# Optimization experiments

Measured on AMD Instinct MI355X. Metric: run time of the kernel, lower is better.

## Reference

```python
import jax, jax.numpy as jnp
import numpy as np

B, T, D, V, SPK = 8, 4096, 512, 1024, 512
DECAY = 0.95
COARSE_SCALE = 0.2
RES_SCALE = 0.35
MAX_LS = 1.2
MAX_SIL = 0.35
COLD_RUNS = 2.0
MIN_DUR = 2.0


def gelu(x):
    return jax.nn.gelu(x, approximate=False)


def setup_inputs() -> dict:
    key = jax.random.key(0)
    ks = jax.random.split(key, 24)
    def n(k, shape, s=1.0):
        return jax.random.normal(k, shape, dtype=jnp.float32) * s
    inp = {}
    inp['content_units'] = jax.random.randint(ks[0], (B, T), 0, V)
    inp['log_anchor'] = n(ks[1], (B, T), 0.5) + 1.0
    inp['unit_mask'] = jax.random.randint(ks[2], (B, T), 0, 2)
    inp['sealed_mask'] = jax.random.randint(ks[3], (B, T), 0, 2)
    inp['silence_mask'] = jax.random.randint(ks[4], (B, T), 0, 2)
    inp['sep_hint'] = jax.random.uniform(ks[5], (B, T), dtype=jnp.float32)
    inp['edge_cue'] = jax.random.uniform(ks[6], (B, T), dtype=jnp.float32)
    inp['run_stability'] = jax.random.uniform(ks[7], (B, T), dtype=jnp.float32)
    inp['global_rate'] = n(ks[8], (B,), 0.1) + 1.0
    inp['local_rate_ema'] = n(ks[9], (B, 1), 0.1) + 1.0
    inp['spk_embed'] = n(ks[10], (B, SPK))
    s = 0.02
    inp['emb_table'] = n(ks[11], (V, D), s)
    inp['feat_W'] = n(ks[12], (5, D), s)      # scalar features -> dim
    inp['feat_b'] = jnp.zeros((D,), jnp.float32)
    inp['spk_W'] = n(ks[13], (SPK, D), s)
    inp['spk_b'] = jnp.zeros((D,), jnp.float32)
    inp['coarse_W1'] = n(ks[14], (D + 1, D), s)
    inp['coarse_b1'] = jnp.zeros((D,), jnp.float32)
    inp['coarse_W2'] = n(ks[15], (D, 1), s)
    inp['coarse_b2'] = jnp.zeros((1,), jnp.float32)
    inp['res_W1'] = n(ks[16], (2 * D + 1, D), s)
    inp['res_b1'] = jnp.zeros((D,), jnp.float32)
    inp['res_W2'] = n(ks[17], (D, 1), s)
    inp['res_b2'] = jnp.zeros((1,), jnp.float32)
    inp['src_rate_init'] = jnp.zeros((1,), jnp.float32)
    return inp


def _local_rate_scan(observed_log, speech_mask, init_rate):
    # Causal masked exponential-decay recurrence: emitted rate at t is the
    # state BEFORE observing step t (strictly causal); state only updates on
    # speech-commit steps.
    def step(rate, xs):
        obs, m = xs  # [B], [B]
        new = jnp.where(m > 0, DECAY * rate + (1.0 - DECAY) * obs, rate)
        return new, rate
    final, seq = jax.lax.scan(step, init_rate, (observed_log.T, speech_mask.T))
    return seq.T, final[:, None]  # [B,T], [B,1]


def reference(content_units, log_anchor, unit_mask, sealed_mask, silence_mask,
              sep_hint, edge_cue, run_stability, global_rate, local_rate_ema,
              spk_embed, emb_table, feat_W, feat_b, spk_W, spk_b,
              coarse_W1, coarse_b1, coarse_W2, coarse_b2,
              res_W1, res_b1, res_W2, res_b2, src_rate_init):
    f32 = jnp.float32
    mask = jnp.clip(unit_mask.astype(f32), 0.0, 1.0)
    sealed = jnp.clip(sealed_mask.astype(f32), 0.0, 1.0)
    silence = jnp.clip(silence_mask.astype(f32), 0.0, 1.0) * mask
    stability = jnp.clip(run_stability.astype(f32), 0.0, 1.0) * mask
    commit = mask * sealed
    sil_commit = commit * silence
    speech = commit * (1.0 - silence)

    la = log_anchor.astype(f32)
    rate_seq, rate_final = _local_rate_scan(la, speech, local_rate_ema[:, 0].astype(f32))

    # CausalUnitRunEncoder: token embedding + projection of per-step scalars
    feats = jnp.stack([la, rate_seq, silence, sep_hint.astype(f32), edge_cue.astype(f32)], axis=-1)  # [B,T,5]
    query = gelu(emb_table[content_units] + feats @ feat_W + feat_b) * mask[..., None]  # [B,T,D]

    grc = global_rate.astype(f32).reshape(-1, 1)[:, :1]  # [B,1]
    spk_ctx = jnp.tanh(spk_embed.astype(f32) @ spk_W + spk_b)  # [B,D]

    gsa = (grc - rate_seq) * commit  # global_shift_analytic [B,T]
    coarse_in = jnp.concatenate([spk_ctx, grc], axis=-1)  # [B,D+1]
    coarse_scalar = COARSE_SCALE * jnp.tanh((gelu(coarse_in @ coarse_W1 + coarse_b1) @ coarse_W2 + coarse_b2)[:, 0])  # [B]
    coarse_corr = coarse_scalar[:, None] * commit
    global_term = (gsa + coarse_corr) * commit

    # residual head: split first-layer weights to avoid materializing the concat
    Wq, Ws, wg = res_W1[:D], res_W1[D:2 * D], res_W1[2 * D]
    h = gelu(query @ Wq + (spk_ctx @ Ws)[:, None, :] + global_term[..., None] * wg + res_b1)  # [B,T,D]
    residual = RES_SCALE * jnp.tanh((h @ res_W2 + res_b2)[..., 0])  # [B,T]

    prefix_prev = jnp.maximum(jnp.cumsum(speech, axis=1) - speech, 0.0)
    cold_gate = jnp.clip(prefix_prev / COLD_RUNS, 0.0, 1.0)
    short_gate = jnp.clip((jnp.maximum(jnp.exp(la), 1.0) - 1.0) / max(1.0, MIN_DUR - 1.0), 0.0, 1.0)
    residual_gate = cold_gate * short_gate * stability * speech
    residual = residual * residual_gate

    pred_speech = jnp.clip(global_term + residual, -MAX_LS, MAX_LS) * speech
    pred_silence = jnp.clip(global_term, -MAX_SIL, MAX_SIL) * sil_commit
    pred = pred_speech + pred_silence  # unit_logstretch [B,T]
    return pred
```

## Files before the change

### kernel.cpp

```cpp
#include <hip/hip_runtime.h>
#include <hip/hip_bf16.h>

#define BB 8
#define TT 4096
#define DD 512
#define MM (BB*TT)
#define DECAYF 0.95f
#define OMDECAYF (1.0f - 0.95f)

typedef __attribute__((ext_vector_type(8))) short bf16x8;
typedef __attribute__((ext_vector_type(4))) float f32x4;

__device__ __forceinline__ float gelu_f(float x){
  return 0.5f * x * (1.0f + erff(x * 0.70710678118654752f));
}

__device__ __forceinline__ unsigned short f2bf(float x){
  unsigned u = __float_as_uint(x);
  unsigned r = (u + 0x7FFFu + ((u >> 16) & 1u)) >> 16;
  return (unsigned short)r;
}

__global__ __launch_bounds__(512) void pre_kernel(
    const float* __restrict__ spk_embed, const float* __restrict__ spk_W,
    const float* __restrict__ spk_b, const float* __restrict__ rW1,
    const float* __restrict__ la_g, const int* __restrict__ um,
    const int* __restrict__ sm, const int* __restrict__ zm,
    const float* __restrict__ stab_g, const float* __restrict__ lre,
    float* __restrict__ spk_ctx, unsigned short* __restrict__ wqt,
    float* __restrict__ rate_seq, float* __restrict__ rgate_a,
    int* __restrict__ active_list, int* __restrict__ acount)
{
  __shared__ float se[DD];
  __shared__ float red[8][64];
  __shared__ float tile[64][65];
  __shared__ float wAg[8], wBg[8], wSg[8];
  __shared__ int wcnt[8];
  int blk = blockIdx.x, t = threadIdx.x;
  int lane = t & 63, wid = t >> 6;

  if (blk < 64){
    int b = blk >> 3, d0 = (blk & 7) * 64;
    int dl = lane, ks = wid;
    se[t] = spk_embed[b*DD + t];
    __syncthreads();
    float a = 0.f;
    const float* wp = spk_W + (long)(ks*64)*DD + d0 + dl;
    #pragma unroll 8
    for (int k = 0; k < 64; ++k) a += se[ks*64 + k] * wp[(long)k*DD];
    red[ks][dl] = a;
    __syncthreads();
    if (t < 64){
      float s = spk_b[d0 + t];
      #pragma unroll
      for (int i = 0; i < 8; ++i) s += red[i][t];
      spk_ctx[b*DD + d0 + t] = tanhf(s);
    }
    return;
  }
  if (blk < 128){
    int tb = blk - 64;
    int nb = (tb & 7) * 64, kb = (tb >> 3) * 64;
    int tx = t & 63, ty = t >> 6;
    #pragma unroll
    for (int i = 0; i < 8; ++i){
      int k = ty + i*8;
      tile[k][tx] = rW1[(long)(kb + k)*DD + nb + tx];
    }
    __syncthreads();
    #pragma unroll
    for (int i = 0; i < 8; ++i){
      int nl = ty + i*8;
      wqt[(long)(nb + nl)*DD + kb + tx] = f2bf(tile[tx][nl]);
    }
    return;
  }

  int b = blk - 128;
  int base = b*TT + t*8;
  float4 la0 = *(const float4*)(la_g + base);
  float4 la1 = *(const float4*)(la_g + base + 4);
  int4 u0 = *(const int4*)(um + base), u1 = *(const int4*)(um + base + 4);
  int4 s0 = *(const int4*)(sm + base), s1 = *(const int4*)(sm + base + 4);
  int4 z0 = *(const int4*)(zm + base), z1 = *(const int4*)(zm + base + 4);
  float4 st0 = *(const float4*)(stab_g + base), st1 = *(const float4*)(stab_g + base + 4);
  float lav[8] = {la0.x,la0.y,la0.z,la0.w,la1.x,la1.y,la1.z,la1.w};
  int uv[8] = {u0.x,u0.y,u0.z,u0.w,u1.x,u1.y,u1.z,u1.w};
  int sv[8] = {s0.x,s0.y,s0.z,s0.w,s1.x,s1.y,s1.z,s1.w};
  int zv[8] = {z0.x,z0.y,z0.z,z0.w,z1.x,z1.y,z1.z,z1.w};
  float stv_[8] = {st0.x,st0.y,st0.z,st0.w,st1.x,st1.y,st1.z,st1.w};
  float spv[8], stv[8];

  float A = 1.f, Bv = 0.f, S = 0.f;
  #pragma unroll
  for (int i = 0; i < 8; ++i){
    float m = uv[i] > 0 ? 1.f : 0.f;
    float sealed = sv[i] > 0 ? 1.f : 0.f;
    float sil = (zv[i] > 0 ? 1.f : 0.f) * m;
    float speech = (m * sealed) * (1.f - sil);
    spv[i] = speech;
    stv[i] = fminf(fmaxf(stv_[i], 0.f), 1.f) * m;
    if (speech > 0.f){
      Bv = DECAYF*Bv + OMDECAYF*lav[i];
      A *= DECAYF;
      S += 1.f;
    }
  }
  #pragma unroll
  for (int d = 1; d < 64; d <<= 1){
    float Au = __shfl_up(A, d, 64);
    float Bu = __shfl_up(Bv, d, 64);
    float Su = __shfl_up(S, d, 64);
    if (lane >= d){ Bv = A*Bu + Bv; A = A*Au; S += Su; }
  }
  if (lane == 63){ wAg[wid] = A; wBg[wid] = Bv; wSg[wid] = S; }
  float Ale = __shfl_up(A, 1, 64), Ble = __shfl_up(Bv, 1, 64), Sle = __shfl_up(S, 1, 64);
  if (lane == 0){ Ale = 1.f; Ble = 0.f; Sle = 0.f; }
  __syncthreads();
  float Awp = 1.f, Bwp = 0.f, Swp = 0.f;
  for (int w = 0; w < wid; ++w){
    Bwp = wAg[w]*Bwp + wBg[w];
    Awp = wAg[w]*Awp;
    Swp += wSg[w];
  }
  float Bex = Ale*Bwp + Ble;
  float Aex = Ale*Awp;
  float Sex = Swp + Sle;

  float rate = Aex*lre[b] + Bex;
  float ps = Sex;
  float ro[8], rg[8];
  #pragma unroll
  for (int i = 0; i < 8; ++i){
    ro[i] = rate;
    float cold = fminf(ps * 0.5f, 1.f);
    float shortg = fminf(fmaxf(expf(lav[i]) - 1.f, 0.f), 1.f);
    rg[i] = cold * shortg * stv[i] * spv[i];
    if (spv[i] > 0.f){
      rate = DECAYF*rate + OMDECAYF*lav[i];
      ps += 1.f;
    }
  }
  *(float4*)(rate_seq + base)     = make_float4(ro[0],ro[1],ro[2],ro[3]);
  *(float4*)(rate_seq + base + 4) = make_float4(ro[4],ro[5],ro[6],ro[7]);
  *(float4*)(rgate_a + base)      = make_float4(rg[0],rg[1],rg[2],rg[3]);
  *(float4*)(rgate_a + base + 4)  = make_float4(rg[4],rg[5],rg[6],rg[7]);

  int nact = 0;
  #pragma unroll
  for (int i = 0; i < 8; ++i) nact += (rg[i] != 0.f) ? 1 : 0;
  int inc = nact;
  #pragma unroll
  for (int d = 1; d < 64; d <<= 1){
    int u = __shfl_up(inc, d, 64);
    if (lane >= d) inc += u;
  }
  int myex = inc - nact;
  if (lane == 63) wcnt[wid] = inc;
  __syncthreads();
  int wbase = 0;
  for (int w = 0; w < wid; ++w) wbase += wcnt[w];
  int pos = wbase + myex;
  int* alist = active_list + b*TT;
  #pragma unroll
  for (int i = 0; i < 8; ++i){
    if (rg[i] != 0.f) alist[pos++] = base + i;
  }
  if (t == 0){
    int total = 0;
    #pragma unroll
    for (int w = 0; w < 8; ++w) total += wcnt[w];
    acount[b] = total;
  }
}

__global__ __launch_bounds__(512) void prep2_kernel(
    const float* __restrict__ spk_ctx, const float* __restrict__ rW1,
    const float* __restrict__ cW1, const float* __restrict__ cb1,
    const float* __restrict__ cW2, const float* __restrict__ grate,
    float* __restrict__ s_vec, float* __restrict__ coarse_part)
{
  __shared__ float sc[DD];
  __shared__ float red1[8][64];
  __shared__ float red2[8][64];
  int blk = blockIdx.x;
  int b = blk >> 3, d0 = (blk & 7) * 64;
  int t = threadIdx.x, dl = t & 63, ks = t >> 6;
  sc[t] = spk_ctx[b*DD + t];
  __syncthreads();
  float a1 = 0.f, a2 = 0.f;
  const float* wsp = rW1 + (long)(DD + ks*64)*DD + d0 + dl;
  const float* wcp = cW1 + (long)(ks*64)*DD + d0 + dl;
  #pragma unroll 4
  for (int k = 0; k < 64; ++k){
    float s = sc[ks*64 + k];
    a1 += s * wsp[(long)k*DD];
    a2 += s * wcp[(long)k*DD];
  }
  red1[ks][dl] = a1; red2[ks][dl] = a2;
  __syncthreads();
  if (t < 64){
    int d = d0 + t;
    float s1 = 0.f;
    float s2 = cb1[d] + grate[b] * cW1[(long)DD*DD + d];
    #pragma unroll
    for (int i = 0; i < 8; ++i){ s1 += red1[i][t]; s2 += red2[i][t]; }
    s_vec[b*DD + d] = s1;
    float hv = gelu_f(s2) * cW2[d];
    #pragma unroll
    for (int sh = 1; sh < 64; sh <<= 1) hv += __shfl_xor(hv, sh, 64);
    if (t == 0) coarse_part[blk] = hv;
  }
}

__global__ __launch_bounds__(512) void main_kernel(
    const int* __restrict__ content, const float* __restrict__ la_g,
    const float* __restrict__ sep, const float* __restrict__ edge,
    const float* __restrict__ emb, const float* __restrict__ fW,
    const float* __restrict__ fb, const float* __restrict__ rate_seq,
    const unsigned short* __restrict__ wqt,
    const float* __restrict__ s_vec, const float* __restrict__ rW1,
    const float* __restrict__ rb1, const float* __restrict__ rW2,
    const float* __restrict__ rb2, const float* __restrict__ grate,
    const float* __restrict__ coarse_part, const float* __restrict__ cb2,
    const int* __restrict__ um, const int* __restrict__ sm,
    const int* __restrict__ zm,
    const float* __restrict__ rgate_a, const int* __restrict__ active_list,
    const int* __restrict__ acount, float* __restrict__ out)
{
  __shared__ unsigned short Af[16*32*32];
  __shared__ unsigned short Bs[3][512*32];
  __shared__ float part[8][32];
  __shared__ int seg_sh[3];
  int blk = blockIdx.x, tid = threadIdx.x, wid = tid >> 6, lane = tid & 63;

  if (blk < 64){
    int gr = blk*512 + tid;
    float rgv = rgate_a[gr];
    if (rgv == 0.f){
      int b = gr >> 12;
      float csum = cb2[0];
      #pragma unroll
      for (int c = 0; c < 8; ++c) csum += coarse_part[b*8 + c];
      float cs = 0.2f * tanhf(csum);
      float m = um[gr] > 0 ? 1.f : 0.f;
      float sealed = sm[gr] > 0 ? 1.f : 0.f;
      float sil = (zm[gr] > 0 ? 1.f : 0.f) * m;
      float commit = m * sealed;
      float speech = commit * (1.f - sil);
      float silc = commit * sil;
      float g = (grate[b] - rate_seq[gr] + cs) * commit;
      out[gr] = fminf(fmaxf(g, -1.2f), 1.2f) * speech
              + fminf(fmaxf(g, -0.35f), 0.35f) * silc;
    }
    return;
  }

  if (tid == 0){
    int p = blk - 64, cum = 0, sb = -1, slo = 0, scnt = 0;
    #pragma unroll
    for (int b = 0; b < BB; ++b){
      int c = acount[b];
      int nb = (c + 31) >> 5;
      if (sb < 0 && p < cum + nb){ sb = b; slo = (p - cum) * 32; scnt = c; }
      cum += nb;
    }
    seg_sh[0] = sb; seg_sh[1] = slo; seg_sh[2] = scnt;
  }
  __syncthreads();
  int seg_b = seg_sh[0], seg_lo = seg_sh[1], seg_cnt = seg_sh[2];
  if (seg_b < 0) return;
  const int* alist = active_list + seg_b*TT;
  const char* wbase = (const char*)wqt;

  float csum = cb2[0];
  #pragma unroll
  for (int c = 0; c < 8; ++c) csum += coarse_part[seg_b*8 + c];
  float cs = 0.2f * tanhf(csum);
  float grc = grate[seg_b];

  auto stageB = [&](unsigned short* dstbuf, int kc){
    int k0b = kc * 64;
    #pragma unroll
    for (int i = 0; i < 4; ++i){
      int j = wid*4 + i;
      int n = j*16 + (lane >> 2);
      int slot = (lane & 3) ^ ((n >> 1) & 3);
      const char* src = wbase + (long)n*1024 + k0b + slot*16;
      char* dst = (char*)dstbuf + j*1024 + (lane << 4);
      __builtin_amdgcn_global_load_lds(
          (const __attribute__((address_space(1))) void*)src,
          (__attribute__((address_space(3))) void*)dst, 16, 0, 0);
    }
  };

  stageB(&Bs[0][0], 0);
  stageB(&Bs[1][0], 1);

  {
    int rr = tid >> 4, kc = tid & 15;
    int p = seg_lo + rr; if (p > seg_cnt-1) p = seg_cnt-1;
    int gr = alist[p];
    float la = la_g[gr], rate = rate_seq[gr];
    float sepv = sep[gr], edgev = edge[gr];
    int k0 = kc * 32;
    const float* er = emb + (long)content[gr]*DD + k0;
    union { bf16x8 v[4]; unsigned short h[32]; } pk;
    #pragma unroll
    for (int i = 0; i < 32; i += 4){
      float4 e  = *(const float4*)(er + i);
      float4 w0 = *(const float4*)(fW + 0*DD + k0 + i);
      float4 w1 = *(const float4*)(fW + 1*DD + k0 + i);
      float4 w3 = *(const float4*)(fW + 3*DD + k0 + i);
      float4 w4 = *(const float4*)(fW + 4*DD + k0 + i);
      float4 bb = *(const float4*)(fb + k0 + i);
      pk.h[i+0] = f2bf(gelu_f(e.x + la*w0.x + rate*w1.x + sepv*w3.x + edgev*w4.x + bb.x));
      pk.h[i+1] = f2bf(gelu_f(e.y + la*w0.y + rate*w1.y + sepv*w3.y + edgev*w4.y + bb.y));
      pk.h[i+2] = f2bf(gelu_f(e.z + la*w0.z + rate*w1.z + sepv*w3.z + edgev*w4.z + bb.z));
      pk.h[i+3] = f2bf(gelu_f(e.w + la*w0.w + rate*w1.w + sepv*w3.w + edgev*w4.w + bb.w));
    }
    int c = (rr >> 1) & 3;
    char* abase = (char*)Af + kc*2048 + rr*64;
    #pragma unroll
    for (int s = 0; s < 4; ++s)
      *(bf16x8*)(abase + ((s ^ c) << 4)) = pk.v[s];
  }
  __syncthreads();

  f32x4 acc[2][4];
  #pragma unroll
  for (int i = 0; i < 2; ++i)
    #pragma unroll
    for (int j = 0; j < 4; ++j) acc[i][j] = (f32x4){0.f,0.f,0.f,0.f};

  int rgp = lane >> 4, li = lane & 15;
  #pragma unroll
  for (int kc = 0; kc < 16; ++kc){
    if (kc > 0){
      if (kc < 15) asm volatile("s_waitcnt vmcnt(4)" ::: "memory");
      else         asm volatile("s_waitcnt vmcnt(0)" ::: "memory");
      __builtin_amdgcn_s_barrier();
      asm volatile("" ::: "memory");
    }
    if (kc + 2 < 16) stageB(&Bs[(kc+2)%3][0], kc+2);
    const char* bsb = (const char*)&Bs[kc%3][0];
    bf16x8 a[2], bb[4];
    #pragma unroll
    for (int mt = 0; mt < 2; ++mt){
      int row = mt*16 + li;
      int slot = rgp ^ ((row >> 1) & 3);
      a[mt] = *(const bf16x8*)((const char*)Af + kc*2048 + row*64 + (slot << 4));
    }
    #pragma unroll
    for (int nt = 0; nt < 4; ++nt){
      int n = wid*64 + nt*16 + li;
      int slot = rgp ^ ((n >> 1) & 3);
      bb[nt] = *(const bf16x8*)(bsb + n*64 + slot*16);
    }
    #pragma unroll
    for (int mt = 0; mt < 2; ++mt)
      #pragma unroll
      for (int nt = 0; nt < 4; ++nt)
        acc[mt][nt] = __builtin_amdgcn_mfma_f32_16x16x32_bf16(a[mt], bb[nt], acc[mt][nt], 0, 0, 0);
  }

  float svv[4], wgv[4], b1v[4], w2v[4];
  #pragma unroll
  for (int nt = 0; nt < 4; ++nt){
    int j = wid*64 + nt*16 + li;
    svv[nt] = s_vec[seg_b*DD + j];
    wgv[nt] = rW1[1024*DD + j];
    b1v[nt] = rb1[j];
    w2v[nt] = rW2[j];
  }
  #pragma unroll
  for (int mt = 0; mt < 2; ++mt){
    #pragma unroll
    for (int r = 0; r < 4; ++r){
      int row = mt*16 + rgp*4 + r;
      int p = seg_lo + row; if (p > seg_cnt-1) p = seg_cnt-1;
      int gr = alist[p];
      float gt = grc - rate_seq[gr] + cs;
      float s = 0.f;
      #pragma unroll
      for (int nt = 0; nt < 4; ++nt){
        float y = acc[mt][nt][r] + svv[nt] + gt*wgv[nt] + b1v[nt];
        s += gelu_f(y) * w2v[nt];
      }
      s += __shfl_xor(s, 1, 64);
      s += __shfl_xor(s, 2, 64);
      s += __shfl_xor(s, 4, 64);
      s += __shfl_xor(s, 8, 64);
      if (li == 0) part[wid][row] = s;
    }
  }
  __syncthreads();
  if (tid < 32){
    int p = seg_lo + tid;
    if (p < seg_cnt){
      int gr = alist[p];
      float s = 0.f;
      #pragma unroll
      for (int w = 0; w < 8; ++w) s += part[w][tid];
      float resid = 0.35f * tanhf(s + rb2[0]) * rgate_a[gr];
      float g = grc - rate_seq[gr] + cs;
      out[gr] = fminf(fmaxf(g + resid, -1.2f), 1.2f);
    }
  }
}

extern "C" void kernel_launch(void* const* d_in, const int* in_sizes, int n_in,
                              void* d_out, int out_size, void* d_ws, size_t ws_size,
                              hipStream_t stream)
{
  const int*   content = (const int*)  d_in[0];
  const float* la      = (const float*)d_in[1];
  const int*   um      = (const int*)  d_in[2];
  const int*   smk     = (const int*)  d_in[3];
  const int*   zm      = (const int*)  d_in[4];
  const float* sep     = (const float*)d_in[5];
  const float* edge    = (const float*)d_in[6];
  const float* stab    = (const float*)d_in[7];
  const float* grate   = (const float*)d_in[8];
  const float* lre     = (const float*)d_in[9];
  const float* spk_e   = (const float*)d_in[10];
  const float* emb     = (const float*)d_in[11];
  const float* fW      = (const float*)d_in[12];
  const float* fb      = (const float*)d_in[13];
  const float* spk_W   = (const float*)d_in[14];
  const float* spk_b   = (const float*)d_in[15];
  const float* cW1     = (const float*)d_in[16];
  const float* cb1     = (const float*)d_in[17];
  const float* cW2     = (const float*)d_in[18];
  const float* cb2     = (const float*)d_in[19];
  const float* rW1     = (const float*)d_in[20];
  const float* rb1     = (const float*)d_in[21];
  const float* rW2     = (const float*)d_in[22];
  const float* rb2     = (const float*)d_in[23];

  char* w = (char*)d_ws;
  unsigned short* wsWqT = (unsigned short*)(w);
  size_t off = 524288;
  float* rate_seq = (float*)(w + off); off += MM*4;
  float* rgate_a  = (float*)(w + off); off += MM*4;
  int*   active_list = (int*)(w + off); off += MM*4;
  float* s_vec    = (float*)(w + off); off += BB*DD*4;
  float* spk_ctx  = (float*)(w + off); off += BB*DD*4;
  float* coarse_part = (float*)(w + off); off += 64*4;
  int*   acount   = (int*)(w + off); off += 256;

  pre_kernel<<<136, 512, 0, stream>>>(spk_e, spk_W, spk_b, rW1,
      la, um, smk, zm, stab, lre,
      spk_ctx, wsWqT, rate_seq, rgate_a, active_list, acount);
  prep2_kernel<<<64, 512, 0, stream>>>(spk_ctx, rW1, cW1, cb1, cW2, grate,
                                       s_vec, coarse_part);
  main_kernel<<<64 + MM/32, 512, 0, stream>>>(content, la, sep, edge, emb, fW, fb,
      rate_seq, wsWqT, s_vec, rW1, rb1, rW2, rb2, grate, coarse_part, cb2,
      um, smk, zm, rgate_a, active_list, acount, (float*)d_out);
}
```

Before: 41.53 us.

## Fuse prep2 into pre_kernel and make main kernel persistent over segments

Each of the 64 speaker blocks in pre_kernel now computes the full speaker context itself, then the s_vec and coarse-head partials. This removes the separate prep2 launch and the spk_ctx round trip through global memory, at the cost of 8x redundant spk_W matvec work per block. main_kernel now launches a fixed 256-block grid that loops over 32-row active segments with stride 256. The inactive-row fill is spread across the first 128 threads of every block. This cuts grid size and launch/tail overhead, but the per-iteration restaging and barriers are serialized within each block.

```diff
diff --git a/kernel.cpp b/kernel.cpp
--- a/kernel.cpp
+++ b/kernel.cpp
@@ -24,15 +24,20 @@
 __global__ __launch_bounds__(512) void pre_kernel(
     const float* __restrict__ spk_embed, const float* __restrict__ spk_W,
     const float* __restrict__ spk_b, const float* __restrict__ rW1,
+    const float* __restrict__ cW1, const float* __restrict__ cb1,
+    const float* __restrict__ cW2, const float* __restrict__ grate,
     const float* __restrict__ la_g, const int* __restrict__ um,
     const int* __restrict__ sm, const int* __restrict__ zm,
     const float* __restrict__ stab_g, const float* __restrict__ lre,
-    float* __restrict__ spk_ctx, unsigned short* __restrict__ wqt,
+    unsigned short* __restrict__ wqt, float* __restrict__ s_vec,
+    float* __restrict__ coarse_part,
     float* __restrict__ rate_seq, float* __restrict__ rgate_a,
     int* __restrict__ active_list, int* __restrict__ acount)
 {
   __shared__ float se[DD];
-  __shared__ float red[8][64];
+  __shared__ float scf[DD];
+  __shared__ float red1[8][64];
+  __shared__ float red2[8][64];
   __shared__ float tile[64][65];
   __shared__ float wAg[8], wBg[8], wSg[8];
   __shared__ int wcnt[8];
@@ -44,17 +49,43 @@
     int dl = lane, ks = wid;
     se[t] = spk_embed[b*DD + t];
     __syncthreads();
-    float a = 0.f;
-    const float* wp = spk_W + (long)(ks*64)*DD + d0 + dl;
-    #pragma unroll 8
-    for (int k = 0; k < 64; ++k) a += se[ks*64 + k] * wp[(long)k*DD];
-    red[ks][dl] = a;
+    for (int dc = 0; dc < 8; ++dc){
+      float a = 0.f;
+      const float* wp = spk_W + (long)(ks*64)*DD + dc*64 + dl;
+      #pragma unroll 8
+      for (int k = 0; k < 64; ++k) a += se[ks*64 + k] * wp[(long)k*DD];
+      red1[ks][dl] = a;
+      __syncthreads();
+      if (t < 64){
+        float s = spk_b[dc*64 + t];
+        #pragma unroll
+        for (int i = 0; i < 8; ++i) s += red1[i][t];
+        scf[dc*64 + t] = tanhf(s);
+      }
+      __syncthreads();
+    }
+    float a1 = 0.f, a2 = 0.f;
+    const float* wsp = rW1 + (long)(DD + ks*64)*DD + d0 + dl;
+    const float* wcp = cW1 + (long)(ks*64)*DD + d0 + dl;
+    #pragma unroll 4
+    for (int k = 0; k < 64; ++k){
+      float s = scf[ks*64 + k];
+      a1 += s * wsp[(long)k*DD];
+      a2 += s * wcp[(long)k*DD];
+    }
+    red1[ks][dl] = a1; red2[ks][dl] = a2;
     __syncthreads();
     if (t < 64){
-      float s = spk_b[d0 + t];
-      #pragma unroll
-      for (int i = 0; i < 8; ++i) s += red[i][t];
-      spk_ctx[b*DD + d0 + t] = tanhf(s);
+      int d = d0 + t;
+      float s1 = 0.f;
+      float s2 = cb1[d] + grate[b] * cW1[(long)DD*DD + d];
+      #pragma unroll
+      for (int i = 0; i < 8; ++i){ s1 += red1[i][t]; s2 += red2[i][t]; }
+      s_vec[b*DD + d] = s1;
+      float hv = gelu_f(s2) * cW2[d];
+      #pragma unroll
+      for (int sh = 1; sh < 64; sh <<= 1) hv += __shfl_xor(hv, sh, 64);
+      if (t == 0) coarse_part[blk] = hv;
     }
     return;
   }
@@ -171,45 +202,6 @@
     #pragma unroll
     for (int w = 0; w < 8; ++w) total += wcnt[w];
     acount[b] = total;
-  }
-}
-
-__global__ __launch_bounds__(512) void prep2_kernel(
-    const float* __restrict__ spk_ctx, const float* __restrict__ rW1,
-    const float* __restrict__ cW1, const float* __restrict__ cb1,
-    const float* __restrict__ cW2, const float* __restrict__ grate,
-    float* __restrict__ s_vec, float* __restrict__ coarse_part)
-{
-  __shared__ float sc[DD];
-  __shared__ float red1[8][64];
-  __shared__ float red2[8][64];
-  int blk = blockIdx.x;
-  int b = blk >> 3, d0 = (blk & 7) * 64;
-  int t = threadIdx.x, dl = t & 63, ks = t >> 6;
-  sc[t] = spk_ctx[b*DD + t];
-  __syncthreads();
-  float a1 = 0.f, a2 = 0.f;
-  const float* wsp = rW1 + (long)(DD + ks*64)*DD + d0 + dl;
-  const float* wcp = cW1 + (long)(ks*64)*DD + d0 + dl;
-  #pragma unroll 4
-  for (int k = 0; k < 64; ++k){
-    float s = sc[ks*64 + k];
-    a1 += s * wsp[(long)k*DD];
-    a2 += s * wcp[(long)k*DD];
-  }
-  red1[ks][dl] = a1; red2[ks][dl] = a2;
-  __syncthreads();
-  if (t < 64){
-    int d = d0 + t;
-    float s1 = 0.f;
-    float s2 = cb1[d] + grate[b] * cW1[(long)DD*DD + d];
-    #pragma unroll
-    for (int i = 0; i < 8; ++i){ s1 += red1[i][t]; s2 += red2[i][t]; }
-    s_vec[b*DD + d] = s1;
-    float hv = gelu_f(s2) * cW2[d];
-    #pragma unroll
-    for (int sh = 1; sh < 64; sh <<= 1) hv += __shfl_xor(hv, sh, 64);
-    if (t == 0) coarse_part[blk] = hv;
   }
 }
 
@@ -231,11 +223,11 @@
   __shared__ unsigned short Af[16*32*32];
   __shared__ unsigned short Bs[3][512*32];
   __shared__ float part[8][32];
-  __shared__ int seg_sh[3];
+  __shared__ int seg_sh[4];
   int blk = blockIdx.x, tid = threadIdx.x, wid = tid >> 6, lane = tid & 63;
 
-  if (blk < 64){
-    int gr = blk*512 + tid;
+  if (tid < 128){
+    int gr = blk*128 + tid;
     float rgv = rgate_a[gr];
     if (rgv == 0.f){
       int b = gr >> 12;
@@ -253,32 +245,9 @@
       out[gr] = fminf(fmaxf(g, -1.2f), 1.2f) * speech
               + fminf(fmaxf(g, -0.35f), 0.35f) * silc;
     }
-    return;
-  }
-
-  if (tid == 0){
-    int p = blk - 64, cum = 0, sb = -1, slo = 0, scnt = 0;
-    #pragma unroll
-    for (int b = 0; b < BB; ++b){
-      int c = acount[b];
-      int nb = (c + 31) >> 5;
-      if (sb < 0 && p < cum + nb){ sb = b; slo = (p - cum) * 32; scnt = c; }
-      cum += nb;
-    }
-    seg_sh[0] = sb; seg_sh[1] = slo; seg_sh[2] = scnt;
-  }
-  __syncthreads();
-  int seg_b = seg_sh[0], seg_lo = seg_sh[1], seg_cnt = seg_sh[2];
-  if (seg_b < 0) return;
-  const int* alist = active_list + seg_b*TT;
+  }
+
   const char* wbase = (const char*)wqt;
-
-  float csum = cb2[0];
-  #pragma unroll
-  for (int c = 0; c < 8; ++c) csum += coarse_part[seg_b*8 + c];
-  float cs = 0.2f * tanhf(csum);
-  float grc = grate[seg_b];
-
   auto stageB = [&](unsigned short* dstbuf, int kc){
     int k0b = kc * 64;
     #pragma unroll
@@ -294,118 +263,143 @@
     }
   };
 
-  stageB(&Bs[0][0], 0);
-  stageB(&Bs[1][0], 1);
-
-  {
-    int rr = tid >> 4, kc = tid & 15;
-    int p = seg_lo + rr; if (p > seg_cnt-1) p = seg_cnt-1;
-    int gr = alist[p];
-    float la = la_g[gr], rate = rate_seq[gr];
-    float sepv = sep[gr], edgev = edge[gr];
-    int k0 = kc * 32;
-    const float* er = emb + (long)content[gr]*DD + k0;
-    union { bf16x8 v[4]; unsigned short h[32]; } pk;
-    #pragma unroll
-    for (int i = 0; i < 32; i += 4){
-      float4 e  = *(const float4*)(er + i);
-      float4 w0 = *(const float4*)(fW + 0*DD + k0 + i);
-      float4 w1 = *(const float4*)(fW + 1*DD + k0 + i);
-      float4 w3 = *(const float4*)(fW + 3*DD + k0 + i);
-      float4 w4 = *(const float4*)(fW + 4*DD + k0 + i);
-      float4 bb = *(const float4*)(fb + k0 + i);
-      pk.h[i+0] = f2bf(gelu_f(e.x + la*w0.x + rate*w1.x + sepv*w3.x + edgev*w4.x + bb.x));
-      pk.h[i+1] = f2bf(gelu_f(e.y + la*w0.y + rate*w1.y + sepv*w3.y + edgev*w4.y + bb.y));
-      pk.h[i+2] = f2bf(gelu_f(e.z + la*w0.z + rate*w1.z + sepv*w3.z + edgev*w4.z + bb.z));
-      pk.h[i+3] = f2bf(gelu_f(e.w + la*w0.w + rate*w1.w + sepv*w3.w + edgev*w4.w + bb.w));
-    }
-    int c = (rr >> 1) & 3;
-    char* abase = (char*)Af + kc*2048 + rr*64;
-    #pragma unroll
-    for (int s = 0; s < 4; ++s)
-      *(bf16x8*)(abase + ((s ^ c) << 4)) = pk.v[s];
-  }
-  __syncthreads();
-
-  f32x4 acc[2][4];
-  #pragma unroll
-  for (int i = 0; i < 2; ++i)
-    #pragma unroll
-    for (int j = 0; j < 4; ++j) acc[i][j] = (f32x4){0.f,0.f,0.f,0.f};
-
-  int rgp = lane >> 4, li = lane & 15;
-  #pragma unroll
-  for (int kc = 0; kc < 16; ++kc){
-    if (kc > 0){
-      if (kc < 15) asm volatile("s_waitcnt vmcnt(4)" ::: "memory");
-      else         asm volatile("s_waitcnt vmcnt(0)" ::: "memory");
-      __builtin_amdgcn_s_barrier();
-      asm volatile("" ::: "memory");
-    }
-    if (kc + 2 < 16) stageB(&Bs[(kc+2)%3][0], kc+2);
-    const char* bsb = (const char*)&Bs[kc%3][0];
-    bf16x8 a[2], bb[4];
+  for (int p = blk; ; p += 256){
+    if (tid == 0){
+      int cum = 0, sb = -1, slo = 0, scnt = 0;
+      #pragma unroll
+      for (int b = 0; b < BB; ++b){
+        int c = acount[b];
+        int nb = (c + 31) >> 5;
+        if (sb < 0 && p < cum + nb){ sb = b; slo = (p - cum) * 32; scnt = c; }
+        cum += nb;
+      }
+      seg_sh[0] = sb; seg_sh[1] = slo; seg_sh[2] = scnt; seg_sh[3] = cum;
+    }
+    __syncthreads();
+    int seg_b = seg_sh[0], seg_lo = seg_sh[1], seg_cnt = seg_sh[2];
+    if (seg_b < 0) break;
+    const int* alist = active_list + seg_b*TT;
+
+    float csum = cb2[0];
+    #pragma unroll
+    for (int c = 0; c < 8; ++c) csum += coarse_part[seg_b*8 + c];
+    float cs = 0.2f * tanhf(csum);
+    float grc = grate[seg_b];
+
+    stageB(&Bs[0][0], 0);
+    stageB(&Bs[1][0], 1);
+
+    {
+      int rr = tid >> 4, kc = tid & 15;
+      int q = seg_lo + rr; if (q > seg_cnt-1) q = seg_cnt-1;
+      int gr = alist[q];
+      float la = la_g[gr], rate = rate_seq[gr];
+      float sepv = sep[gr], edgev = edge[gr];
+      int k0 = kc * 32;
+      const float* er = emb + (long)content[gr]*DD + k0;
+      union { bf16x8 v[4]; unsigned short h[32]; } pk;
+      #pragma unroll
+      for (int i = 0; i < 32; i += 4){
+        float4 e  = *(const float4*)(er + i);
+        float4 w0 = *(const float4*)(fW + 0*DD + k0 + i);
+        float4 w1 = *(const float4*)(fW + 1*DD + k0 + i);
+        float4 w3 = *(const float4*)(fW + 3*DD + k0 + i);
+        float4 w4 = *(const float4*)(fW + 4*DD + k0 + i);
+        float4 bb = *(const float4*)(fb + k0 + i);
+        pk.h[i+0] = f2bf(gelu_f(e.x + la*w0.x + rate*w1.x + sepv*w3.x + edgev*w4.x + bb.x));
+        pk.h[i+1] = f2bf(gelu_f(e.y + la*w0.y + rate*w1.y + sepv*w3.y + edgev*w4.y + bb.y));
+        pk.h[i+2] = f2bf(gelu_f(e.z + la*w0.z + rate*w1.z + sepv*w3.z + edgev*w4.z + bb.z));
+        pk.h[i+3] = f2bf(gelu_f(e.w + la*w0.w + rate*w1.w + sepv*w3.w + edgev*w4.w + bb.w));
+      }
+      int c = (rr >> 1) & 3;
+      char* abase = (char*)Af + kc*2048 + rr*64;
+      #pragma unroll
+      for (int s = 0; s < 4; ++s)
+        *(bf16x8*)(abase + ((s ^ c) << 4)) = pk.v[s];
+    }
+    __syncthreads();
+
+    f32x4 acc[2][4];
+    #pragma unroll
+    for (int i = 0; i < 2; ++i)
+      #pragma unroll
+      for (int j = 0; j < 4; ++j) acc[i][j] = (f32x4){0.f,0.f,0.f,0.f};
+
+    int rgp = lane >> 4, li = lane & 15;
+    #pragma unroll
+    for (int kc = 0; kc < 16; ++kc){
+      if (kc > 0){
+        if (kc < 15) asm volatile("s_waitcnt vmcnt(4)" ::: "memory");
+        else         asm volatile("s_waitcnt vmcnt(0)" ::: "memory");
+        __builtin_amdgcn_s_barrier();
+        asm volatile("" ::: "memory");
+      }
+      if (kc + 2 < 16) stageB(&Bs[(kc+2)%3][0], kc+2);
+      const char* bsb = (const char*)&Bs[kc%3][0];
+      bf16x8 a[2], bb[4];
+      #pragma unroll
+      for (int mt = 0; mt < 2; ++mt){
+        int row = mt*16 + li;
+        int slot = rgp ^ ((row >> 1) & 3);
+        a[mt] = *(const bf16x8*)((const char*)Af + kc*2048 + row*64 + (slot << 4));
+      }
+      #pragma unroll
+      for (int nt = 0; nt < 4; ++nt){
+        int n = wid*64 + nt*16 + li;
+        int slot = rgp ^ ((n >> 1) & 3);
+        bb[nt] = *(const bf16x8*)(bsb + n*64 + slot*16);
+      }
+      #pragma unroll
+      for (int mt = 0; mt < 2; ++mt)
+        #pragma unroll
+        for (int nt = 0; nt < 4; ++nt)
+          acc[mt][nt] = __builtin_amdgcn_mfma_f32_16x16x32_bf16(a[mt], bb[nt], acc[mt][nt], 0, 0, 0);
+    }
+
+    float svv[4], wgv[4], b1v[4], w2v[4];
+    #pragma unroll
+    for (int nt = 0; nt < 4; ++nt){
+      int j = wid*64 + nt*16 + li;
+      svv[nt] = s_vec[seg_b*DD + j];
+      wgv[nt] = rW1[1024*DD + j];
+      b1v[nt] = rb1[j];
+      w2v[nt] = rW2[j];
+    }
     #pragma unroll
     for (int mt = 0; mt < 2; ++mt){
-      int row = mt*16 + li;
-      int slot = rgp ^ ((row >> 1) & 3);
-      a[mt] = *(const bf16x8*)((const char*)Af + kc*2048 + row*64 + (slot << 4));
-    }
-    #pragma unroll
-    for (int nt = 0; nt < 4; ++nt){
-      int n = wid*64 + nt*16 + li;
-      int slot = rgp ^ ((n >> 1) & 3);
-      bb[nt] = *(const bf16x8*)(bsb + n*64 + slot*16);
-    }
-    #pragma unroll
-    for (int mt = 0; mt < 2; ++mt)
-      #pragma unroll
-      for (int nt = 0; nt < 4; ++nt)
-        acc[mt][nt] = __builtin_amdgcn_mfma_f32_16x16x32_bf16(a[mt], bb[nt], acc[mt][nt], 0, 0, 0);
-  }
-
-  float svv[4], wgv[4], b1v[4], w2v[4];
-  #pragma unroll
-  for (int nt = 0; nt < 4; ++nt){
-    int j = wid*64 + nt*16 + li;
-    svv[nt] = s_vec[seg_b*DD + j];
-    wgv[nt] = rW1[1024*DD + j];
-    b1v[nt] = rb1[j];
-    w2v[nt] = rW2[j];
-  }
-  #pragma unroll
-  for (int mt = 0; mt < 2; ++mt){
-    #pragma unroll
-    for (int r = 0; r < 4; ++r){
-      int row = mt*16 + rgp*4 + r;
-      int p = seg_lo + row; if (p > seg_cnt-1) p = seg_cnt-1;
-      int gr = alist[p];
-      float gt = grc - rate_seq[gr] + cs;
-      float s = 0.f;
-      #pragma unroll
-      for (int nt = 0; nt < 4; ++nt){
-        float y = acc[mt][nt][r] + svv[nt] + gt*wgv[nt] + b1v[nt];
-        s += gelu_f(y) * w2v[nt];
-      }
-      s += __shfl_xor(s, 1, 64);
-      s += __shfl_xor(s, 2, 64);
-      s += __shfl_xor(s, 4, 64);
-      s += __shfl_xor(s, 8, 64);
-      if (li == 0) part[wid][row] = s;
-    }
-  }
-  __syncthreads();
-  if (tid < 32){
-    int p = seg_lo + tid;
-    if (p < seg_cnt){
-      int gr = alist[p];
-      float s = 0.f;
-      #pragma unroll
-      for (int w = 0; w < 8; ++w) s += part[w][tid];
-      float resid = 0.35f * tanhf(s + rb2[0]) * rgate_a[gr];
-      float g = grc - rate_seq[gr] + cs;
-      out[gr] = fminf(fmaxf(g + resid, -1.2f), 1.2f);
-    }
+      #pragma unroll
+      for (int r = 0; r < 4; ++r){
+        int row = mt*16 + rgp*4 + r;
+        int q = seg_lo + row; if (q > seg_cnt-1) q = seg_cnt-1;
+        int gr = alist[q];
+        float gt = grc - rate_seq[gr] + cs;
+        float s = 0.f;
+        #pragma unroll
+        for (int nt = 0; nt < 4; ++nt){
+          float y = acc[mt][nt][r] + svv[nt] + gt*wgv[nt] + b1v[nt];
+          s += gelu_f(y) * w2v[nt];
+        }
+        s += __shfl_xor(s, 1, 64);
+        s += __shfl_xor(s, 2, 64);
+        s += __shfl_xor(s, 4, 64);
+        s += __shfl_xor(s, 8, 64);
+        if (li == 0) part[wid][row] = s;
+      }
+    }
+    __syncthreads();
+    if (tid < 32){
+      int q = seg_lo + tid;
+      if (q < seg_cnt){
+        int gr = alist[q];
+        float s = 0.f;
+        #pragma unroll
+        for (int w = 0; w < 8; ++w) s += part[w][tid];
+        float resid = 0.35f * tanhf(s + rb2[0]) * rgate_a[gr];
+        float g = grc - rate_seq[gr] + cs;
+        out[gr] = fminf(fmaxf(g + resid, -1.2f), 1.2f);
+      }
+    }
+    __syncthreads();
   }
 }
 
@@ -445,16 +439,13 @@
   float* rgate_a  = (float*)(w + off); off += MM*4;
   int*   active_list = (int*)(w + off); off += MM*4;
   float* s_vec    = (float*)(w + off); off += BB*DD*4;
-  float* spk_ctx  = (float*)(w + off); off += BB*DD*4;
   float* coarse_part = (float*)(w + off); off += 64*4;
   int*   acount   = (int*)(w + off); off += 256;
 
-  pre_kernel<<<136, 512, 0, stream>>>(spk_e, spk_W, spk_b, rW1,
-      la, um, smk, zm, stab, lre,
-      spk_ctx, wsWqT, rate_seq, rgate_a, active_list, acount);
-  prep2_kernel<<<64, 512, 0, stream>>>(spk_ctx, rW1, cW1, cb1, cW2, grate,
-                                       s_vec, coarse_part);
-  main_kernel<<<64 + MM/32, 512, 0, stream>>>(content, la, sep, edge, emb, fW, fb,
+  pre_kernel<<<136, 512, 0, stream>>>(spk_e, spk_W, spk_b, rW1, cW1, cb1, cW2,
+      grate, la, um, smk, zm, stab, lre,
+      wsWqT, s_vec, coarse_part, rate_seq, rgate_a, active_list, acount);
+  main_kernel<<<256, 512, 0, stream>>>(content, la, sep, edge, emb, fW, fb,
       rate_seq, wsWqT, s_vec, rW1, rb1, rW2, rb2, grate, coarse_part, cb2,
       um, smk, zm, rgate_a, active_list, acount, (float*)d_out);
 }
```

After: 76.75 us. 1.85x slower.

## Make main kernel persistent with grid-stride tiles and double-buffered per-wave B staging

Applied to the files above, without the earlier changes.

The main kernel now launches 256 blocks and loops over 32-row active tiles with a stride of 256, instead of launching one block per possible tile plus 64 dedicated fast-path blocks. The inactive-row fast path is spread across the first 128 threads of every block. B staging drops from three LDS buffers to two and removes the per-k-step block barrier, relying on each wave reading only the weight rows it loaded itself. This cuts launch and empty-block overhead and per-k-step sync. In exchange there is less prefetch depth, one block per CU running serial tiles, and a reliance on wave-private LDS ordering.

```diff
diff --git a/kernel.cpp b/kernel.cpp
--- a/kernel.cpp
+++ b/kernel.cpp
@@ -229,13 +229,13 @@
     const int* __restrict__ acount, float* __restrict__ out)
 {
   __shared__ unsigned short Af[16*32*32];
-  __shared__ unsigned short Bs[3][512*32];
+  __shared__ unsigned short Bs[2][512*32];
   __shared__ float part[8][32];
   __shared__ int seg_sh[3];
   int blk = blockIdx.x, tid = threadIdx.x, wid = tid >> 6, lane = tid & 63;
 
-  if (blk < 64){
-    int gr = blk*512 + tid;
+  if (tid < 128){
+    int gr = blk*128 + tid;
     float rgv = rgate_a[gr];
     if (rgv == 0.f){
       int b = gr >> 12;
@@ -253,32 +253,9 @@
       out[gr] = fminf(fmaxf(g, -1.2f), 1.2f) * speech
               + fminf(fmaxf(g, -0.35f), 0.35f) * silc;
     }
-    return;
-  }
-
-  if (tid == 0){
-    int p = blk - 64, cum = 0, sb = -1, slo = 0, scnt = 0;
-    #pragma unroll
-    for (int b = 0; b < BB; ++b){
-      int c = acount[b];
-      int nb = (c + 31) >> 5;
-      if (sb < 0 && p < cum + nb){ sb = b; slo = (p - cum) * 32; scnt = c; }
-      cum += nb;
-    }
-    seg_sh[0] = sb; seg_sh[1] = slo; seg_sh[2] = scnt;
-  }
-  __syncthreads();
-  int seg_b = seg_sh[0], seg_lo = seg_sh[1], seg_cnt = seg_sh[2];
-  if (seg_b < 0) return;
-  const int* alist = active_list + seg_b*TT;
+  }
+
   const char* wbase = (const char*)wqt;
-
-  float csum = cb2[0];
-  #pragma unroll
-  for (int c = 0; c < 8; ++c) csum += coarse_part[seg_b*8 + c];
-  float cs = 0.2f * tanhf(csum);
-  float grc = grate[seg_b];
-
   auto stageB = [&](unsigned short* dstbuf, int kc){
     int k0b = kc * 64;
     #pragma unroll
@@ -294,118 +271,138 @@
     }
   };
 
-  stageB(&Bs[0][0], 0);
-  stageB(&Bs[1][0], 1);
-
-  {
-    int rr = tid >> 4, kc = tid & 15;
-    int p = seg_lo + rr; if (p > seg_cnt-1) p = seg_cnt-1;
-    int gr = alist[p];
-    float la = la_g[gr], rate = rate_seq[gr];
-    float sepv = sep[gr], edgev = edge[gr];
-    int k0 = kc * 32;
-    const float* er = emb + (long)content[gr]*DD + k0;
-    union { bf16x8 v[4]; unsigned short h[32]; } pk;
-    #pragma unroll
-    for (int i = 0; i < 32; i += 4){
-      float4 e  = *(const float4*)(er + i);
-      float4 w0 = *(const float4*)(fW + 0*DD + k0 + i);
-      float4 w1 = *(const float4*)(fW + 1*DD + k0 + i);
-      float4 w3 = *(const float4*)(fW + 3*DD + k0 + i);
-      float4 w4 = *(const float4*)(fW + 4*DD + k0 + i);
-      float4 bb = *(const float4*)(fb + k0 + i);
-      pk.h[i+0] = f2bf(gelu_f(e.x + la*w0.x + rate*w1.x + sepv*w3.x + edgev*w4.x + bb.x));
-      pk.h[i+1] = f2bf(gelu_f(e.y + la*w0.y + rate*w1.y + sepv*w3.y + edgev*w4.y + bb.y));
-      pk.h[i+2] = f2bf(gelu_f(e.z + la*w0.z + rate*w1.z + sepv*w3.z + edgev*w4.z + bb.z));
-      pk.h[i+3] = f2bf(gelu_f(e.w + la*w0.w + rate*w1.w + sepv*w3.w + edgev*w4.w + bb.w));
-    }
-    int c = (rr >> 1) & 3;
-    char* abase = (char*)Af + kc*2048 + rr*64;
-    #pragma unroll
-    for (int s = 0; s < 4; ++s)
-      *(bf16x8*)(abase + ((s ^ c) << 4)) = pk.v[s];
-  }
-  __syncthreads();
-
-  f32x4 acc[2][4];
-  #pragma unroll
-  for (int i = 0; i < 2; ++i)
-    #pragma unroll
-    for (int j = 0; j < 4; ++j) acc[i][j] = (f32x4){0.f,0.f,0.f,0.f};
-
-  int rgp = lane >> 4, li = lane & 15;
-  #pragma unroll
-  for (int kc = 0; kc < 16; ++kc){
-    if (kc > 0){
+  for (int p = blk; ; p += 256){
+    if (tid == 0){
+      int cum = 0, sb = -1, slo = 0, scnt = 0;
+      #pragma unroll
+      for (int b = 0; b < BB; ++b){
+        int c = acount[b];
+        int nb = (c + 31) >> 5;
+        if (sb < 0 && p < cum + nb){ sb = b; slo = (p - cum) * 32; scnt = c; }
+        cum += nb;
+      }
+      seg_sh[0] = sb; seg_sh[1] = slo; seg_sh[2] = scnt;
+    }
+    __syncthreads();
+    int seg_b = seg_sh[0], seg_lo = seg_sh[1], seg_cnt = seg_sh[2];
+    if (seg_b < 0) break;
+    const int* alist = active_list + seg_b*TT;
+
+    float csum = cb2[0];
+    #pragma unroll
+    for (int c = 0; c < 8; ++c) csum += coarse_part[seg_b*8 + c];
+    float cs = 0.2f * tanhf(csum);
+    float grc = grate[seg_b];
+
+    stageB(&Bs[0][0], 0);
+
+    {
+      int rr = tid >> 4, kc = tid & 15;
+      int q = seg_lo + rr; if (q > seg_cnt-1) q = seg_cnt-1;
+      int gr = alist[q];
+      float la = la_g[gr], rate = rate_seq[gr];
+      float sepv = sep[gr], edgev = edge[gr];
+      int k0 = kc * 32;
+      const float* er = emb + (long)content[gr]*DD + k0;
+      union { bf16x8 v[4]; unsigned short h[32]; } pk;
+      #pragma unroll
+      for (int i = 0; i < 32; i += 4){
+        float4 e  = *(const float4*)(er + i);
+        float4 w0 = *(const float4*)(fW + 0*DD + k0 + i);
+        float4 w1 = *(const float4*)(fW + 1*DD + k0 + i);
+        float4 w3 = *(const float4*)(fW + 3*DD + k0 + i);
+        float4 w4 = *(const float4*)(fW + 4*DD + k0 + i);
+        float4 bb = *(const float4*)(fb + k0 + i);
+        pk.h[i+0] = f2bf(gelu_f(e.x + la*w0.x + rate*w1.x + sepv*w3.x + edgev*w4.x + bb.x));
+        pk.h[i+1] = f2bf(gelu_f(e.y + la*w0.y + rate*w1.y + sepv*w3.y + edgev*w4.y + bb.y));
+        pk.h[i+2] = f2bf(gelu_f(e.z + la*w0.z + rate*w1.z + sepv*w3.z + edgev*w4.z + bb.z));
+        pk.h[i+3] = f2bf(gelu_f(e.w + la*w0.w + rate*w1.w + sepv*w3.w + edgev*w4.w + bb.w));
+      }
+      int c = (rr >> 1) & 3;
+      char* abase = (char*)Af + kc*2048 + rr*64;
+      #pragma unroll
+      for (int s = 0; s < 4; ++s)
+        *(bf16x8*)(abase + ((s ^ c) << 4)) = pk.v[s];
+    }
+    __syncthreads();
+
+    f32x4 acc[2][4];
+    #pragma unroll
+    for (int i = 0; i < 2; ++i)
+      #pragma unroll
+      for (int j = 0; j < 4; ++j) acc[i][j] = (f32x4){0.f,0.f,0.f,0.f};
+
+    int rgp = lane >> 4, li = lane & 15;
+    #pragma unroll
+    for (int kc = 0; kc < 16; ++kc){
+      if (kc < 15) stageB(&Bs[(kc+1)&1][0], kc+1);
       if (kc < 15) asm volatile("s_waitcnt vmcnt(4)" ::: "memory");
       else         asm volatile("s_waitcnt vmcnt(0)" ::: "memory");
-      __builtin_amdgcn_s_barrier();
-      asm volatile("" ::: "memory");
-    }
-    if (kc + 2 < 16) stageB(&Bs[(kc+2)%3][0], kc+2);
-    const char* bsb = (const char*)&Bs[kc%3][0];
-    bf16x8 a[2], bb[4];
+      const char* bsb = (const char*)&Bs[kc&1][0];
+      bf16x8 a[2], bb[4];
+      #pragma unroll
+      for (int mt = 0; mt < 2; ++mt){
+        int row = mt*16 + li;
+        int slot = rgp ^ ((row >> 1) & 3);
+        a[mt] = *(const bf16x8*)((const char*)Af + kc*2048 + row*64 + (slot << 4));
+      }
+      #pragma unroll
+      for (int nt = 0; nt < 4; ++nt){
+        int n = wid*64 + nt*16 + li;
+        int slot = rgp ^ ((n >> 1) & 3);
+        bb[nt] = *(const bf16x8*)(bsb + n*64 + slot*16);
+      }
+      #pragma unroll
+      for (int mt = 0; mt < 2; ++mt)
+        #pragma unroll
+        for (int nt = 0; nt < 4; ++nt)
+          acc[mt][nt] = __builtin_amdgcn_mfma_f32_16x16x32_bf16(a[mt], bb[nt], acc[mt][nt], 0, 0, 0);
+    }
+
+    float svv[4], wgv[4], b1v[4], w2v[4];
+    #pragma unroll
+    for (int nt = 0; nt < 4; ++nt){
+      int j = wid*64 + nt*16 + li;
+      svv[nt] = s_vec[seg_b*DD + j];
+      wgv[nt] = rW1[1024*DD + j];
+      b1v[nt] = rb1[j];
+      w2v[nt] = rW2[j];
+    }
     #pragma unroll
     for (int mt = 0; mt < 2; ++mt){
-      int row = mt*16 + li;
-      int slot = rgp ^ ((row >> 1) & 3);
-      a[mt] = *(const bf16x8*)((const char*)Af + kc*2048 + row*64 + (slot << 4));
-    }
-    #pragma unroll
-    for (int nt = 0; nt < 4; ++nt){
-      int n = wid*64 + nt*16 + li;
-      int slot = rgp ^ ((n >> 1) & 3);
-      bb[nt] = *(const bf16x8*)(bsb + n*64 + slot*16);
-    }
-    #pragma unroll
-    for (int mt = 0; mt < 2; ++mt)
-      #pragma unroll
-      for (int nt = 0; nt < 4; ++nt)
-        acc[mt][nt] = __builtin_amdgcn_mfma_f32_16x16x32_bf16(a[mt], bb[nt], acc[mt][nt], 0, 0, 0);
-  }
-
-  float svv[4], wgv[4], b1v[4], w2v[4];
-  #pragma unroll
-  for (int nt = 0; nt < 4; ++nt){
-    int j = wid*64 + nt*16 + li;
-    svv[nt] = s_vec[seg_b*DD + j];
-    wgv[nt] = rW1[1024*DD + j];
-    b1v[nt] = rb1[j];
-    w2v[nt] = rW2[j];
-  }
-  #pragma unroll
-  for (int mt = 0; mt < 2; ++mt){
-    #pragma unroll
-    for (int r = 0; r < 4; ++r){
-      int row = mt*16 + rgp*4 + r;
-      int p = seg_lo + row; if (p > seg_cnt-1) p = seg_cnt-1;
-      int gr = alist[p];
-      float gt = grc - rate_seq[gr] + cs;
-      float s = 0.f;
-      #pragma unroll
-      for (int nt = 0; nt < 4; ++nt){
-        float y = acc[mt][nt][r] + svv[nt] + gt*wgv[nt] + b1v[nt];
-        s += gelu_f(y) * w2v[nt];
-      }
-      s += __shfl_xor(s, 1, 64);
-      s += __shfl_xor(s, 2, 64);
-      s += __shfl_xor(s, 4, 64);
-      s += __shfl_xor(s, 8, 64);
-      if (li == 0) part[wid][row] = s;
-    }
-  }
-  __syncthreads();
-  if (tid < 32){
-    int p = seg_lo + tid;
-    if (p < seg_cnt){
-      int gr = alist[p];
-      float s = 0.f;
-      #pragma unroll
-      for (int w = 0; w < 8; ++w) s += part[w][tid];
-      float resid = 0.35f * tanhf(s + rb2[0]) * rgate_a[gr];
-      float g = grc - rate_seq[gr] + cs;
-      out[gr] = fminf(fmaxf(g + resid, -1.2f), 1.2f);
-    }
+      #pragma unroll
+      for (int r = 0; r < 4; ++r){
+        int row = mt*16 + rgp*4 + r;
+        int q = seg_lo + row; if (q > seg_cnt-1) q = seg_cnt-1;
+        int gr = alist[q];
+        float gt = grc - rate_seq[gr] + cs;
+        float s = 0.f;
+        #pragma unroll
+        for (int nt = 0; nt < 4; ++nt){
+          float y = acc[mt][nt][r] + svv[nt] + gt*wgv[nt] + b1v[nt];
+          s += gelu_f(y) * w2v[nt];
+        }
+        s += __shfl_xor(s, 1, 64);
+        s += __shfl_xor(s, 2, 64);
+        s += __shfl_xor(s, 4, 64);
+        s += __shfl_xor(s, 8, 64);
+        if (li == 0) part[wid][row] = s;
+      }
+    }
+    __syncthreads();
+    if (tid < 32){
+      int q = seg_lo + tid;
+      if (q < seg_cnt){
+        int gr = alist[q];
+        float s = 0.f;
+        #pragma unroll
+        for (int w = 0; w < 8; ++w) s += part[w][tid];
+        float resid = 0.35f * tanhf(s + rb2[0]) * rgate_a[gr];
+        float g = grc - rate_seq[gr] + cs;
+        out[gr] = fminf(fmaxf(g + resid, -1.2f), 1.2f);
+      }
+    }
+    __syncthreads();
   }
 }
 
@@ -454,7 +451,7 @@
       spk_ctx, wsWqT, rate_seq, rgate_a, active_list, acount);
   prep2_kernel<<<64, 512, 0, stream>>>(spk_ctx, rW1, cW1, cb1, cW2, grate,
                                        s_vec, coarse_part);
-  main_kernel<<<64 + MM/32, 512, 0, stream>>>(content, la, sep, edge, emb, fW, fb,
+  main_kernel<<<256, 512, 0, stream>>>(content, la, sep, edge, emb, fW, fb,
       rate_seq, wsWqT, s_vec, rW1, rb1, rW2, rb2, grate, coarse_part, cb2,
       um, smk, zm, rgate_a, active_list, acount, (float*)d_out);
 }
```

Measured after the change: 50.79 us. +22.3%, slower.
